# Optimization experiments

Measured on AMD Instinct MI355X. Metric: run time of the kernel, lower is better.

Reference implementation:

```python
import jax, jax.numpy as jnp
import numpy as np
import math

DIM = 768
NUM_HEADS = 12
HEAD_DIM = DIM // NUM_HEADS


def setup_inputs() -> dict:
    key = jax.random.key(0)
    k_x, k_q, k_k, k_v = jax.random.split(key, 4)
    s = 1.0 / math.sqrt(DIM)
    return {
        "x": jax.random.normal(k_x, (2, 2048, DIM), dtype=jnp.float32),
        "Wq": jax.random.normal(k_q, (DIM, DIM), dtype=jnp.float32) * s,
        "Wk": jax.random.normal(k_k, (DIM, DIM), dtype=jnp.float32) * s,
        "Wv": jax.random.normal(k_v, (DIM, DIM), dtype=jnp.float32) * s,
    }


def reference(x, Wq, Wk, Wv):
    b, n, _ = x.shape
    # nn.Linear(dim, dim, bias=False): y = x @ W.T
    def split_heads(y):
        return y.reshape(b, n, NUM_HEADS, HEAD_DIM).transpose(0, 2, 1, 3)  # b h n d
    Q = split_heads(x @ Wq.T)
    K = split_heads(x @ Wk.T)
    V = split_heads(x @ Wv.T)
    scores = jnp.einsum('bhqd,bhkd->bhqk', Q, K)
    # FAITHFUL to source: softmax over the HEADS axis (dim=1), then scale by 1/sqrt(dim)
    attn = jax.nn.softmax(scores, axis=1) / math.sqrt(DIM)
    out = jnp.einsum('bhqk,bhkd->bhqd', attn, V)
    out = out.transpose(0, 2, 1, 3).reshape(b, n, DIM)  # b n (h d)
    return out  # to_out is Identity (project_out=False)
```

## Files before the change

kernel.cpp:

```cpp
#include <hip/hip_runtime.h>

#define DIM 768
#define NHEADS 12
#define HDIM 64
#define BATCH 2
#define SEQ 2048
#define ROWS (BATCH*SEQ)
#define KSPLIT 4

typedef __attribute__((ext_vector_type(8))) _Float16 f16x8;
typedef __attribute__((ext_vector_type(4))) _Float16 f16x4;
typedef __attribute__((ext_vector_type(2))) _Float16 f16x2;
typedef __attribute__((ext_vector_type(4))) float    f32x4;

__device__ __forceinline__ void dma16(const _Float16* g, _Float16* l) {
    __builtin_amdgcn_global_load_lds(
        (const __attribute__((address_space(1))) unsigned int*)g,
        (__attribute__((address_space(3))) unsigned int*)l, 16, 0, 0);
}


__global__ __launch_bounds__(256) void cvt_all(
    const float* __restrict__ x,  const float* __restrict__ wq,
    const float* __restrict__ wk, const float* __restrict__ wv,
    _Float16* __restrict__ xf,  _Float16* __restrict__ wqf,
    _Float16* __restrict__ wkf, _Float16* __restrict__ wvf)
{
    const int lane = threadIdx.x & 63;
    const int wid  = (blockIdx.x * 256 + threadIdx.x) >> 6;
    const float* src; _Float16* dst; int t;
    if (wid < 6144)      { src = x;  dst = xf;  t = wid;        }
    else if (wid < 7296) { src = wq; dst = wqf; t = wid - 6144; }
    else if (wid < 8448) { src = wk; dst = wkf; t = wid - 7296; }
    else                 { src = wv; dst = wvf; t = wid - 8448; }
    const int c = lane & 15, quad = lane >> 4;
    const int mt = t / 24, kt = t % 24;
    const float* p = src + (size_t)(mt*16 + c) * 768 + kt*32 + quad*8;
    float4 v0 = *(const float4*)p;
    float4 v1 = *(const float4*)(p + 4);
    f16x8 o;
    o[0]=(_Float16)v0.x; o[1]=(_Float16)v0.y; o[2]=(_Float16)v0.z; o[3]=(_Float16)v0.w;
    o[4]=(_Float16)v1.x; o[5]=(_Float16)v1.y; o[6]=(_Float16)v1.z; o[7]=(_Float16)v1.w;
    *reinterpret_cast<f16x8*>(dst + ((size_t)t * 64 + lane) * 8) = o;
}

__global__ __launch_bounds__(256) void gemm3(
    const _Float16* __restrict__ xf, const _Float16* __restrict__ wqkf,
    const _Float16* __restrict__ wvf,
    _Float16* __restrict__ Qf, _Float16* __restrict__ Kf, _Float16* __restrict__ Vkt)
{
    __shared__ _Float16 Ab[2][8*512];
    __shared__ _Float16 Bb[2][8*512];
    const int tid = threadIdx.x, lane = tid & 63, w = tid >> 6;
    const int c = lane & 15, quad = lane >> 4;

    const _Float16 *Af, *Bf;
    int mt0, nt0, mode;
    if ((int)blockIdx.x < 384) {
        int mt = blockIdx.x / 12, nt = blockIdx.x % 12;
        Af = xf; Bf = wqkf; mt0 = mt*8; nt0 = nt*8; mode = 0;
    } else {
        int v = blockIdx.x - 384;
        int mt = v / 32, nt = v % 32;
        Af = wvf; Bf = xf; mt0 = mt*8; nt0 = nt*8; mode = 1;
    }

    auto stage = [&](int kt, int buf) {
#pragma unroll
        for (int u = 0; u < 4; ++u) {
            const int cc = w*4 + u;
            const _Float16* s = (cc < 8) ? Af + ((size_t)(mt0+cc)*24 + kt)*512
                                         : Bf + ((size_t)(nt0+cc-8)*24 + kt)*512;
            _Float16* d = (cc < 8) ? &Ab[buf][cc*512] : &Bb[buf][(cc-8)*512];
            dma16(s + lane*8, d);
        }
    };

    stage(0, 0);
    __syncthreads();

    f32x4 acc[4][4] = {};
    for (int kt = 0; kt < 24; ++kt) {
        const int cur = kt & 1;
        if (kt < 23) stage(kt+1, cur^1);
        f16x8 a[4], b[4];
#pragma unroll
        for (int i = 0; i < 4; ++i)
            a[i] = *(const f16x8*)(&Ab[cur][((w>>1)*4 + i)*512] + lane*8);
#pragma unroll
        for (int j = 0; j < 4; ++j)
            b[j] = *(const f16x8*)(&Bb[cur][((w&1)*4 + j)*512] + lane*8);
#pragma unroll
        for (int i = 0; i < 4; ++i)
#pragma unroll
            for (int j = 0; j < 4; ++j)
                acc[i][j] = __builtin_amdgcn_mfma_f32_16x16x32_f16(a[i], b[j], acc[i][j], 0,0,0);
        __syncthreads();
    }

    _Float16* L = &Ab[0][0] + w*1280;
#pragma unroll
    for (int i2 = 0; i2 < 2; ++i2)
#pragma unroll
        for (int j2 = 0; j2 < 2; ++j2) {
#pragma unroll
            for (int ii = 0; ii < 2; ++ii)
#pragma unroll
                for (int jj = 0; jj < 2; ++jj)
#pragma unroll
                    for (int r = 0; r < 4; ++r)
                        L[(ii*16 + quad*4 + r)*40 + jj*16 + c] =
                            (_Float16)acc[i2*2+ii][j2*2+jj][r];
#pragma unroll
            for (int ii = 0; ii < 2; ++ii) {
                const int mtg = mt0 + (w>>1)*4 + i2*2 + ii;
                if (mode == 0) {
                    f16x8 v = *(const f16x8*)(L + (ii*16 + c)*40 + quad*8);
                    const int nt32 = (nt0 + (w&1)*4)/2 + j2;
                    _Float16* dst = (nt32 < 24)
                        ? Qf + ((size_t)(mtg*24 + nt32)*64 + lane)*8
                        : Kf + ((size_t)(mtg*24 + nt32 - 24)*64 + lane)*8;
                    *(f16x8*)dst = v;
                } else {
#pragma unroll
                    for (int jj = 0; jj < 2; ++jj) {
                        f16x4 v4 = *(const f16x4*)(L + (ii*16 + c)*40 + jj*16 + quad*4);
                        const int kcu = nt0 + (w&1)*4 + j2*2 + jj;
                        *(f16x4*)(Vkt + ((size_t)kcu*48 + mtg)*256 + lane*4) = v4;
                    }
                }
            }
        }
}

__global__ __launch_bounds__(1024) __attribute__((amdgpu_waves_per_eu(4)))
void attn_kernel(
    const _Float16* __restrict__ Qf, const _Float16* __restrict__ Kf,
    const _Float16* __restrict__ Vkt,
    float* __restrict__ out,
    _Float16* __restrict__ part)
{
    __shared__ _Float16 Kb[24*512];
    __shared__ _Float16 Vb[48*256];
    __shared__ _Float16 Sr[4*12*320];
    __shared__ _Float16 Pl[4*12*320];
    const int tid = threadIdx.x, lane = tid & 63, w = tid >> 6;
    const int c = lane & 15, quad = lane >> 4;
    const int qi = w >> 2, g = w & 3;

    const int bid = blockIdx.x;
    const int qb = bid & 31;
    const int ks = (bid >> 5) & 3;
    const int b  = bid >> 7;
    const int qrow0 = b*SEQ + qb*64;
    const int qt16  = (qrow0 >> 4) + qi;
    const int kb16  = (b*SEQ + ks*(SEQ/KSPLIT)) >> 4;

    f16x8 qreg[6];
#pragma unroll
    for (int u = 0; u < 6; ++u)
        qreg[u] = *(const f16x8*)(Qf + ((size_t)(qt16*24 + g*6 + u)*64 + lane)*8);

    if (w < 8) {
#pragma unroll
        for (int u = 0; u < 3; ++u)
            dma16(Kf + ((size_t)kb16*24 + w*3 + u)*512 + lane*8, &Kb[(w*3+u)*512]);
    }
    __syncthreads();

    f32x4 o_acc[12] = {};

    for (int t = 0; t < 32; ++t) {
        f32x4 s3[3];
#pragma unroll
        for (int hh = 0; hh < 3; ++hh) {
            f16x8 ka = *(const f16x8*)(&Kb[(g*6 + hh*2    )*512] + lane*8);
            f16x8 k2 = *(const f16x8*)(&Kb[(g*6 + hh*2 + 1)*512] + lane*8);
            f32x4 a = {};
            a = __builtin_amdgcn_mfma_f32_16x16x32_f16(qreg[hh*2],   ka, a, 0,0,0);
            a = __builtin_amdgcn_mfma_f32_16x16x32_f16(qreg[hh*2+1], k2, a, 0,0,0);
            s3[hh] = a;
        }
#pragma unroll
        for (int hh = 0; hh < 3; ++hh)
#pragma unroll
            for (int r = 0; r < 4; ++r)
                Sr[(qi*12 + g*3 + hh)*320 + (quad*4 + r)*20 + c] = (_Float16)s3[hh][r];
        if (t > 0) {
#pragma unroll
            for (int h = 0; h < 12; ++h) {
                f16x4 pf = *(const f16x4*)(Pl + (qi*12 + h)*320 + c*20 + quad*4);
                f16x4 vv = *(const f16x4*)(Vb + (h*4 + g)*256 + lane*4);
                o_acc[h] = __builtin_amdgcn_mfma_f32_16x16x16f16(pf, vv, o_acc[h], 0,0,0);
            }
        }
        __syncthreads();
        if (w >= 8) {
#pragma unroll
            for (int u = 0; u < 3; ++u)
                dma16(Vkt + (size_t)(kb16+t)*12288 + ((w-8)*3+u)*512 + lane*8,
                      &Vb[((w-8)*3+u)*512]);
        } else if (t < 31) {
#pragma unroll
            for (int u = 0; u < 3; ++u)
                dma16(Kf + ((size_t)(kb16+t+1)*24 + w*3 + u)*512 + lane*8,
                      &Kb[(w*3+u)*512]);
        }
        {
            float e[12];
#pragma unroll
            for (int h = 0; h < 12; ++h)
                e[h] = __expf((float)Sr[(qi*12 + h)*320 + (quad*4 + g)*20 + c]);
            float s01 = e[0]+e[1], s23 = e[2]+e[3], s45 = e[4]+e[5];
            float s67 = e[6]+e[7], s89 = e[8]+e[9], sab = e[10]+e[11];
            float sum = ((s01+s23)+(s45+s67)) + (s89+sab);
            const float inv = 1.0f / (sum * 27.712812921102035f);
#pragma unroll
            for (int h = 0; h < 12; ++h)
                Pl[(qi*12 + h)*320 + (quad*4 + g)*20 + c] = (_Float16)(e[h]*inv);
        }
        __syncthreads();
    }
#pragma unroll
    for (int h = 0; h < 12; ++h) {
        f16x4 pf = *(const f16x4*)(Pl + (qi*12 + h)*320 + c*20 + quad*4);
        f16x4 vv = *(const f16x4*)(Vb + (h*4 + g)*256 + lane*4);
        o_acc[h] = __builtin_amdgcn_mfma_f32_16x16x16f16(pf, vv, o_acc[h], 0,0,0);
    }

    if (ks == 0) {
#pragma unroll
        for (int h = 0; h < 12; ++h) {
            const int col = h*64 + g*16 + c;
#pragma unroll
            for (int r = 0; r < 4; ++r)
                out[(size_t)(qrow0 + qi*16 + quad*4 + r) * DIM + col] = o_acc[h][r];
        }
    } else {
        _Float16* dst = part + (size_t)(ks - 1) * ROWS * DIM;
#pragma unroll
        for (int h = 0; h < 12; ++h) {
            const int col = h*64 + g*16 + c;
#pragma unroll
            for (int r = 0; r < 4; ++r)
                dst[(size_t)(qrow0 + qi*16 + quad*4 + r) * DIM + col] =
                    (_Float16)o_acc[h][r];
        }
    }
}

__global__ __launch_bounds__(256) void reduce_add4(
    float* __restrict__ out, const _Float16* __restrict__ part, int n4)
{
    int i = blockIdx.x * 256 + threadIdx.x;
    if (i >= n4) return;
    float4 o = reinterpret_cast<float4*>(out)[i];
    const size_t N = (size_t)ROWS * DIM;
#pragma unroll
    for (int p = 0; p < 3; ++p) {
        f16x4 v = reinterpret_cast<const f16x4*>(part + p * N)[i];
        o.x += (float)v[0]; o.y += (float)v[1]; o.z += (float)v[2]; o.w += (float)v[3];
    }
    reinterpret_cast<float4*>(out)[i] = o;
}

extern "C" void kernel_launch(void* const* d_in, const int* in_sizes, int n_in,
                              void* d_out, int out_size, void* d_ws, size_t ws_size,
                              hipStream_t stream)
{
    const float* x  = (const float*)d_in[0];
    const float* Wq = (const float*)d_in[1];
    const float* Wk = (const float*)d_in[2];
    const float* Wv = (const float*)d_in[3];

    _Float16* ws  = (_Float16*)d_ws;
    const size_t XS = (size_t)ROWS * DIM;
    const size_t WS = (size_t)DIM * DIM;
    _Float16* xf   = ws;
    _Float16* wqf  = xf  + XS;
    _Float16* wkf  = wqf + WS;
    _Float16* wvf  = wkf + WS;
    _Float16* Qf   = wvf + WS;
    _Float16* Kf   = Qf  + XS;
    _Float16* Vkt  = Kf  + XS;
    _Float16* part = Vkt + XS;

    cvt_all<<<2400, 256, 0, stream>>>(x, Wq, Wk, Wv, xf, wqf, wkf, wvf);
    gemm3<<<576, 256, 0, stream>>>(xf, wqf, wvf, Qf, Kf, Vkt);
    attn_kernel<<<BATCH * KSPLIT * 32, 1024, 0, stream>>>(
        Qf, Kf, Vkt, (float*)d_out, part);
    reduce_add4<<<(int)(XS/4 + 255)/256, 256, 0, stream>>>(
        (float*)d_out, part, (int)(XS/4));
}
```

Before: 190.3 us.

## Fuse exp into score MFMA, split softmax sum via LDS partials, load V from global

Swaps the MFMA operand order so each lane holds score values in a transposed layout. Exponentials are computed directly from registers, and only per-wave partial sums go to LDS, replacing the full fp16 score round-trip through shared memory. V tiles are loaded straight from global memory into registers, split across iterations, instead of being staged through LDS by dedicated waves. K loading is spread over 12 waves, and output stores become vectorized row-contiguous writes. The trade is more register pressure and uncached global V loads on the critical path, in exchange for less LDS traffic and fewer conversions.

```diff
diff --git a/kernel.cpp b/kernel.cpp
--- a/kernel.cpp
+++ b/kernel.cpp
@@ -140,10 +140,9 @@
     float* __restrict__ out,
     _Float16* __restrict__ part)
 {
-    __shared__ _Float16 Kb[24*512];
-    __shared__ _Float16 Vb[48*256];
-    __shared__ _Float16 Sr[4*12*320];
-    __shared__ _Float16 Pl[4*12*320];
+    __shared__ __attribute__((aligned(16))) _Float16 Kb[24*512];
+    __shared__ __attribute__((aligned(16))) float    Ps[16][16][20];
+    __shared__ __attribute__((aligned(16))) _Float16 Pl[4][12][16][20];
     const int tid = threadIdx.x, lane = tid & 63, w = tid >> 6;
     const int c = lane & 15, quad = lane >> 4;
     const int qi = w >> 2, g = w & 3;
@@ -161,90 +160,99 @@
     for (int u = 0; u < 6; ++u)
         qreg[u] = *(const f16x8*)(Qf + ((size_t)(qt16*24 + g*6 + u)*64 + lane)*8);
 
-    if (w < 8) {
-#pragma unroll
-        for (int u = 0; u < 3; ++u)
-            dma16(Kf + ((size_t)kb16*24 + w*3 + u)*512 + lane*8, &Kb[(w*3+u)*512]);
+    const _Float16* Vb0 = Vkt + ((size_t)kb16*48 + g)*256 + lane*4;
+
+    if (w < 12) {
+#pragma unroll
+        for (int u = 0; u < 2; ++u)
+            dma16(Kf + ((size_t)kb16*24 + w*2 + u)*512 + lane*8, &Kb[(w*2+u)*512]);
     }
     __syncthreads();
 
     f32x4 o_acc[12] = {};
+    f16x4 vv[12];
+    f32x4 e3[3];
 
     for (int t = 0; t < 32; ++t) {
-        f32x4 s3[3];
 #pragma unroll
         for (int hh = 0; hh < 3; ++hh) {
             f16x8 ka = *(const f16x8*)(&Kb[(g*6 + hh*2    )*512] + lane*8);
             f16x8 k2 = *(const f16x8*)(&Kb[(g*6 + hh*2 + 1)*512] + lane*8);
             f32x4 a = {};
-            a = __builtin_amdgcn_mfma_f32_16x16x32_f16(qreg[hh*2],   ka, a, 0,0,0);
-            a = __builtin_amdgcn_mfma_f32_16x16x32_f16(qreg[hh*2+1], k2, a, 0,0,0);
-            s3[hh] = a;
-        }
-#pragma unroll
-        for (int hh = 0; hh < 3; ++hh)
+            a = __builtin_amdgcn_mfma_f32_16x16x32_f16(ka, qreg[hh*2],   a, 0,0,0);
+            a = __builtin_amdgcn_mfma_f32_16x16x32_f16(k2, qreg[hh*2+1], a, 0,0,0);
+            f32x4 ee;
+#pragma unroll
+            for (int r = 0; r < 4; ++r) ee[r] = __expf(a[r]);
+            e3[hh] = ee;
+        }
+        {
+            f32x4 ps;
+#pragma unroll
+            for (int r = 0; r < 4; ++r) ps[r] = e3[0][r] + e3[1][r] + e3[2][r];
+            *(f32x4*)&Ps[qi*4+g][c][quad*4] = ps;
+        }
+        if (t > 0) {
+#pragma unroll
+            for (int h = 6; h < 12; ++h)
+                vv[h] = *(const f16x4*)(Vb0 + ((size_t)(t-1)*48 + h*4)*256);
+#pragma unroll
+            for (int h = 0; h < 12; ++h) {
+                f16x4 pf = *(const f16x4*)&Pl[qi][h][c][quad*4];
+                o_acc[h] = __builtin_amdgcn_mfma_f32_16x16x16f16(vv[h], pf, o_acc[h], 0,0,0);
+            }
+        }
+        __syncthreads();
+        if (w < 12 && t < 31) {
+#pragma unroll
+            for (int u = 0; u < 2; ++u)
+                dma16(Kf + ((size_t)(kb16+t+1)*24 + w*2 + u)*512 + lane*8,
+                      &Kb[(w*2+u)*512]);
+        }
+        {
+            f32x4 s0 = *(const f32x4*)&Ps[qi*4+0][c][quad*4];
+            f32x4 s1 = *(const f32x4*)&Ps[qi*4+1][c][quad*4];
+            f32x4 s2 = *(const f32x4*)&Ps[qi*4+2][c][quad*4];
+            f32x4 s3 = *(const f32x4*)&Ps[qi*4+3][c][quad*4];
+            f32x4 inv;
 #pragma unroll
             for (int r = 0; r < 4; ++r)
-                Sr[(qi*12 + g*3 + hh)*320 + (quad*4 + r)*20 + c] = (_Float16)s3[hh][r];
-        if (t > 0) {
-#pragma unroll
-            for (int h = 0; h < 12; ++h) {
-                f16x4 pf = *(const f16x4*)(Pl + (qi*12 + h)*320 + c*20 + quad*4);
-                f16x4 vv = *(const f16x4*)(Vb + (h*4 + g)*256 + lane*4);
-                o_acc[h] = __builtin_amdgcn_mfma_f32_16x16x16f16(pf, vv, o_acc[h], 0,0,0);
+                inv[r] = 1.0f / ((s0[r]+s1[r]+s2[r]+s3[r]) * 27.712812921102035f);
+#pragma unroll
+            for (int hh = 0; hh < 3; ++hh) {
+                f16x4 pw;
+#pragma unroll
+                for (int r = 0; r < 4; ++r) pw[r] = (_Float16)(e3[hh][r]*inv[r]);
+                *(f16x4*)&Pl[qi][g*3+hh][c][quad*4] = pw;
             }
         }
+#pragma unroll
+        for (int h = 0; h < 6; ++h)
+            vv[h] = *(const f16x4*)(Vb0 + ((size_t)t*48 + h*4)*256);
         __syncthreads();
-        if (w >= 8) {
-#pragma unroll
-            for (int u = 0; u < 3; ++u)
-                dma16(Vkt + (size_t)(kb16+t)*12288 + ((w-8)*3+u)*512 + lane*8,
-                      &Vb[((w-8)*3+u)*512]);
-        } else if (t < 31) {
-#pragma unroll
-            for (int u = 0; u < 3; ++u)
-                dma16(Kf + ((size_t)(kb16+t+1)*24 + w*3 + u)*512 + lane*8,
-                      &Kb[(w*3+u)*512]);
-        }
-        {
-            float e[12];
-#pragma unroll
-            for (int h = 0; h < 12; ++h)
-                e[h] = __expf((float)Sr[(qi*12 + h)*320 + (quad*4 + g)*20 + c]);
-            float s01 = e[0]+e[1], s23 = e[2]+e[3], s45 = e[4]+e[5];
-            float s67 = e[6]+e[7], s89 = e[8]+e[9], sab = e[10]+e[11];
-            float sum = ((s01+s23)+(s45+s67)) + (s89+sab);
-            const float inv = 1.0f / (sum * 27.712812921102035f);
-#pragma unroll
-            for (int h = 0; h < 12; ++h)
-                Pl[(qi*12 + h)*320 + (quad*4 + g)*20 + c] = (_Float16)(e[h]*inv);
-        }
-        __syncthreads();
-    }
+    }
+#pragma unroll
+    for (int h = 6; h < 12; ++h)
+        vv[h] = *(const f16x4*)(Vb0 + ((size_t)31*48 + h*4)*256);
 #pragma unroll
     for (int h = 0; h < 12; ++h) {
-        f16x4 pf = *(const f16x4*)(Pl + (qi*12 + h)*320 + c*20 + quad*4);
-        f16x4 vv = *(const f16x4*)(Vb + (h*4 + g)*256 + lane*4);
-        o_acc[h] = __builtin_amdgcn_mfma_f32_16x16x16f16(pf, vv, o_acc[h], 0,0,0);
+        f16x4 pf = *(const f16x4*)&Pl[qi][h][c][quad*4];
+        o_acc[h] = __builtin_amdgcn_mfma_f32_16x16x16f16(vv[h], pf, o_acc[h], 0,0,0);
     }
 
     if (ks == 0) {
 #pragma unroll
-        for (int h = 0; h < 12; ++h) {
-            const int col = h*64 + g*16 + c;
-#pragma unroll
-            for (int r = 0; r < 4; ++r)
-                out[(size_t)(qrow0 + qi*16 + quad*4 + r) * DIM + col] = o_acc[h][r];
-        }
+        for (int h = 0; h < 12; ++h)
+            *(f32x4*)(out + (size_t)(qrow0 + qi*16 + c)*DIM + h*64 + g*16 + quad*4)
+                = o_acc[h];
     } else {
         _Float16* dst = part + (size_t)(ks - 1) * ROWS * DIM;
 #pragma unroll
         for (int h = 0; h < 12; ++h) {
-            const int col = h*64 + g*16 + c;
-#pragma unroll
-            for (int r = 0; r < 4; ++r)
-                dst[(size_t)(qrow0 + qi*16 + quad*4 + r) * DIM + col] =
-                    (_Float16)o_acc[h][r];
+            f16x4 v;
+#pragma unroll
+            for (int r = 0; r < 4; ++r) v[r] = (_Float16)o_acc[h][r];
+            *(f16x4*)(dst + (size_t)(qrow0 + qi*16 + c)*DIM + h*64 + g*16 + quad*4) = v;
         }
     }
 }
```

Result: no change. 188.6 us (-0.9%).

## Restructure attention kernel: register-resident Q, direct global K/V loads, swizzled P buffer

Applied to the files above, without the earlier changes.

Rewrites the attention kernel to use 512-thread blocks over 32 query rows. Each wave holds all 24 Q fragments in registers and streams K and V straight from global memory, dropping the LDS staging of K and V. Softmax across heads is computed in registers with max-subtraction and exp2, made possible by folding log2(e) into Wq during fp16 conversion. Probabilities go through a swizzled LDS buffer, and each wave accumulates three heads, so output is written as vector stores. This trades LDS traffic and barriers for more global/L2 loads and much higher register pressure (24 Q fragments), which may limit occupancy.

```diff
diff --git a/kernel.cpp b/kernel.cpp
--- a/kernel.cpp
+++ b/kernel.cpp
@@ -19,6 +19,10 @@
         (__attribute__((address_space(3))) unsigned int*)l, 16, 0, 0);
 }
 
+__device__ __forceinline__ void barrier_lgkm() {
+    asm volatile("s_waitcnt lgkmcnt(0)\n\ts_barrier" ::: "memory");
+}
+
 
 __global__ __launch_bounds__(256) void cvt_all(
     const float* __restrict__ x,  const float* __restrict__ wq,
@@ -29,8 +33,9 @@
     const int lane = threadIdx.x & 63;
     const int wid  = (blockIdx.x * 256 + threadIdx.x) >> 6;
     const float* src; _Float16* dst; int t;
+    float sc = 1.0f;
     if (wid < 6144)      { src = x;  dst = xf;  t = wid;        }
-    else if (wid < 7296) { src = wq; dst = wqf; t = wid - 6144; }
+    else if (wid < 7296) { src = wq; dst = wqf; t = wid - 6144; sc = 1.4426950408889634f; }
     else if (wid < 8448) { src = wk; dst = wkf; t = wid - 7296; }
     else                 { src = wv; dst = wvf; t = wid - 8448; }
     const int c = lane & 15, quad = lane >> 4;
@@ -39,8 +44,8 @@
     float4 v0 = *(const float4*)p;
     float4 v1 = *(const float4*)(p + 4);
     f16x8 o;
-    o[0]=(_Float16)v0.x; o[1]=(_Float16)v0.y; o[2]=(_Float16)v0.z; o[3]=(_Float16)v0.w;
-    o[4]=(_Float16)v1.x; o[5]=(_Float16)v1.y; o[6]=(_Float16)v1.z; o[7]=(_Float16)v1.w;
+    o[0]=(_Float16)(v0.x*sc); o[1]=(_Float16)(v0.y*sc); o[2]=(_Float16)(v0.z*sc); o[3]=(_Float16)(v0.w*sc);
+    o[4]=(_Float16)(v1.x*sc); o[5]=(_Float16)(v1.y*sc); o[6]=(_Float16)(v1.z*sc); o[7]=(_Float16)(v1.w*sc);
     *reinterpret_cast<f16x8*>(dst + ((size_t)t * 64 + lane) * 8) = o;
 }
 
@@ -133,119 +138,110 @@
         }
 }
 
-__global__ __launch_bounds__(1024) __attribute__((amdgpu_waves_per_eu(4)))
+__global__ __launch_bounds__(512)
 void attn_kernel(
     const _Float16* __restrict__ Qf, const _Float16* __restrict__ Kf,
     const _Float16* __restrict__ Vkt,
     float* __restrict__ out,
     _Float16* __restrict__ part)
 {
-    __shared__ _Float16 Kb[24*512];
-    __shared__ _Float16 Vb[48*256];
-    __shared__ _Float16 Sr[4*12*320];
-    __shared__ _Float16 Pl[4*12*320];
+    __shared__ __attribute__((aligned(16))) _Float16 Pl[2][4][12][256];
     const int tid = threadIdx.x, lane = tid & 63, w = tid >> 6;
     const int c = lane & 15, quad = lane >> 4;
-    const int qi = w >> 2, g = w & 3;
+    const int qi = w >> 2, x = w & 3;
 
     const int bid = blockIdx.x;
-    const int qb = bid & 31;
-    const int ks = (bid >> 5) & 3;
-    const int b  = bid >> 7;
-    const int qrow0 = b*SEQ + qb*64;
+    const int qb = bid & 63;
+    const int ks = (bid >> 6) & 3;
+    const int b  = bid >> 8;
+    const int qrow0 = b*SEQ + qb*32;
     const int qt16  = (qrow0 >> 4) + qi;
     const int kb16  = (b*SEQ + ks*(SEQ/KSPLIT)) >> 4;
 
-    f16x8 qreg[6];
-#pragma unroll
-    for (int u = 0; u < 6; ++u)
-        qreg[u] = *(const f16x8*)(Qf + ((size_t)(qt16*24 + g*6 + u)*64 + lane)*8);
-
-    if (w < 8) {
-#pragma unroll
-        for (int u = 0; u < 3; ++u)
-            dma16(Kf + ((size_t)kb16*24 + w*3 + u)*512 + lane*8, &Kb[(w*3+u)*512]);
-    }
-    __syncthreads();
-
-    f32x4 o_acc[12] = {};
-
-    for (int t = 0; t < 32; ++t) {
-        f32x4 s3[3];
-#pragma unroll
-        for (int hh = 0; hh < 3; ++hh) {
-            f16x8 ka = *(const f16x8*)(&Kb[(g*6 + hh*2    )*512] + lane*8);
-            f16x8 k2 = *(const f16x8*)(&Kb[(g*6 + hh*2 + 1)*512] + lane*8);
-            f32x4 a = {};
-            a = __builtin_amdgcn_mfma_f32_16x16x32_f16(qreg[hh*2],   ka, a, 0,0,0);
-            a = __builtin_amdgcn_mfma_f32_16x16x32_f16(qreg[hh*2+1], k2, a, 0,0,0);
-            s3[hh] = a;
-        }
+    const int ploff = c*16 + ((quad ^ (c >> 2)) << 2);
+
+    f16x8 qreg[24];
+#pragma unroll
+    for (int f = 0; f < 24; ++f)
+        qreg[f] = *(const f16x8*)(Qf + ((size_t)(qt16*24 + f)*64 + lane)*8);
+
+    f32x4 o_acc[3][4] = {};
+
+    for (int t = 0; t < 8; ++t) {
+        const _Float16* Kp = Kf + ((size_t)(kb16 + t*4 + x)*24*64)*8 + (size_t)lane*8;
+        f16x4 s16[12];
+        f32x4 m = {-3e38f, -3e38f, -3e38f, -3e38f};
+#pragma unroll
+        for (int h = 0; h < 12; ++h) {
+            f16x8 k0 = *(const f16x8*)(Kp + (2*h    )*512);
+            f16x8 k1 = *(const f16x8*)(Kp + (2*h + 1)*512);
+            f32x4 s = {};
+            s = __builtin_amdgcn_mfma_f32_16x16x32_f16(k0, qreg[2*h    ], s, 0,0,0);
+            s = __builtin_amdgcn_mfma_f32_16x16x32_f16(k1, qreg[2*h + 1], s, 0,0,0);
+#pragma unroll
+            for (int r = 0; r < 4; ++r) {
+                m[r] = fmaxf(m[r], s[r]);
+                s16[h][r] = (_Float16)s[r];
+            }
+        }
+        f32x4 sum = {};
+#pragma unroll
+        for (int h = 0; h < 12; ++h) {
+#pragma unroll
+            for (int r = 0; r < 4; ++r) {
+                float e = __builtin_amdgcn_exp2f((float)s16[h][r] - m[r]);
+                sum[r] += e;
+                s16[h][r] = (_Float16)e;
+            }
+        }
+        f16x4 inv16;
+#pragma unroll
+        for (int r = 0; r < 4; ++r)
+            inv16[r] = (_Float16)__builtin_amdgcn_rcpf(sum[r] * 27.712812921102035f);
+        {
+            _Float16* wp = &Pl[qi][x][0][0] + ploff;
+#pragma unroll
+            for (int h = 0; h < 12; ++h)
+                *(f16x4*)(wp + h*256) = s16[h] * inv16;
+        }
+        barrier_lgkm();
+
+        const int h0 = 3*x;
+        const _Float16* Vp = Vkt + (size_t)(kb16 + t*4)*48*256 + (size_t)lane*4;
+#pragma unroll
+        for (int ksi = 0; ksi < 4; ++ksi) {
+#pragma unroll
+            for (int hh = 0; hh < 3; ++hh) {
+                f16x4 pf = *(const f16x4*)(&Pl[qi][ksi][h0+hh][0] + ploff);
+#pragma unroll
+                for (int dt = 0; dt < 4; ++dt) {
+                    f16x4 vv = *(const f16x4*)(Vp + ((size_t)ksi*48 + (h0+hh)*4 + dt)*256);
+                    o_acc[hh][dt] = __builtin_amdgcn_mfma_f32_16x16x16f16(vv, pf, o_acc[hh][dt], 0,0,0);
+                }
+            }
+        }
+        barrier_lgkm();
+    }
+
+    const int orow = qrow0 + qi*16 + c;
+    if (ks == 0) {
 #pragma unroll
         for (int hh = 0; hh < 3; ++hh)
 #pragma unroll
-            for (int r = 0; r < 4; ++r)
-                Sr[(qi*12 + g*3 + hh)*320 + (quad*4 + r)*20 + c] = (_Float16)s3[hh][r];
-        if (t > 0) {
-#pragma unroll
-            for (int h = 0; h < 12; ++h) {
-                f16x4 pf = *(const f16x4*)(Pl + (qi*12 + h)*320 + c*20 + quad*4);
-                f16x4 vv = *(const f16x4*)(Vb + (h*4 + g)*256 + lane*4);
-                o_acc[h] = __builtin_amdgcn_mfma_f32_16x16x16f16(pf, vv, o_acc[h], 0,0,0);
-            }
-        }
-        __syncthreads();
-        if (w >= 8) {
-#pragma unroll
-            for (int u = 0; u < 3; ++u)
-                dma16(Vkt + (size_t)(kb16+t)*12288 + ((w-8)*3+u)*512 + lane*8,
-                      &Vb[((w-8)*3+u)*512]);
-        } else if (t < 31) {
-#pragma unroll
-            for (int u = 0; u < 3; ++u)
-                dma16(Kf + ((size_t)(kb16+t+1)*24 + w*3 + u)*512 + lane*8,
-                      &Kb[(w*3+u)*512]);
-        }
-        {
-            float e[12];
-#pragma unroll
-            for (int h = 0; h < 12; ++h)
-                e[h] = __expf((float)Sr[(qi*12 + h)*320 + (quad*4 + g)*20 + c]);
-            float s01 = e[0]+e[1], s23 = e[2]+e[3], s45 = e[4]+e[5];
-            float s67 = e[6]+e[7], s89 = e[8]+e[9], sab = e[10]+e[11];
-            float sum = ((s01+s23)+(s45+s67)) + (s89+sab);
-            const float inv = 1.0f / (sum * 27.712812921102035f);
-#pragma unroll
-            for (int h = 0; h < 12; ++h)
-                Pl[(qi*12 + h)*320 + (quad*4 + g)*20 + c] = (_Float16)(e[h]*inv);
-        }
-        __syncthreads();
-    }
-#pragma unroll
-    for (int h = 0; h < 12; ++h) {
-        f16x4 pf = *(const f16x4*)(Pl + (qi*12 + h)*320 + c*20 + quad*4);
-        f16x4 vv = *(const f16x4*)(Vb + (h*4 + g)*256 + lane*4);
-        o_acc[h] = __builtin_amdgcn_mfma_f32_16x16x16f16(pf, vv, o_acc[h], 0,0,0);
-    }
-
-    if (ks == 0) {
-#pragma unroll
-        for (int h = 0; h < 12; ++h) {
-            const int col = h*64 + g*16 + c;
-#pragma unroll
-            for (int r = 0; r < 4; ++r)
-                out[(size_t)(qrow0 + qi*16 + quad*4 + r) * DIM + col] = o_acc[h][r];
-        }
+            for (int dt = 0; dt < 4; ++dt)
+                *(f32x4*)(out + (size_t)orow*DIM + (3*x+hh)*64 + dt*16 + quad*4)
+                    = o_acc[hh][dt];
     } else {
         _Float16* dst = part + (size_t)(ks - 1) * ROWS * DIM;
 #pragma unroll
-        for (int h = 0; h < 12; ++h) {
-            const int col = h*64 + g*16 + c;
-#pragma unroll
-            for (int r = 0; r < 4; ++r)
-                dst[(size_t)(qrow0 + qi*16 + quad*4 + r) * DIM + col] =
-                    (_Float16)o_acc[h][r];
-        }
+        for (int hh = 0; hh < 3; ++hh)
+#pragma unroll
+            for (int dt = 0; dt < 4; ++dt) {
+                f16x4 v;
+#pragma unroll
+                for (int r = 0; r < 4; ++r) v[r] = (_Float16)o_acc[hh][dt][r];
+                *(f16x4*)(dst + (size_t)orow*DIM + (3*x+hh)*64 + dt*16 + quad*4) = v;
+            }
     }
 }
 
@@ -287,7 +283,7 @@
 
     cvt_all<<<2400, 256, 0, stream>>>(x, Wq, Wk, Wv, xf, wqf, wkf, wvf);
     gemm3<<<576, 256, 0, stream>>>(xf, wqf, wvf, Qf, Kf, Vkt);
-    attn_kernel<<<BATCH * KSPLIT * 32, 1024, 0, stream>>>(
+    attn_kernel<<<BATCH * KSPLIT * 64, 512, 0, stream>>>(
         Qf, Kf, Vkt, (float*)d_out, part);
     reduce_add4<<<(int)(XS/4 + 255)/256, 256, 0, stream>>>(
         (float*)d_out, part, (int)(XS/4));
```

Result: slower. 240.6 us (+26.4%).
